# Kernel tuning notes

Measured on AMD Instinct MI355X. Metric: run time of the kernel, lower is better.

Reference implementation:

```python
import jax, jax.numpy as jnp
import numpy as np

T, B, H, W_IMG = 8, 4, 128, 128
NUM_CLS = 21
LEAK = 0.99   # config.leak_mem
THR = 1.0     # config.def_threshold
EPS = 1e-4    # BatchNorm2d eps


@jax.custom_vjp
def spike(mem):
    # Heaviside spike with 'Linear' surrogate gradient
    return (mem > THR).astype(mem.dtype)

def _spike_fwd(mem):
    return spike(mem), mem

def _spike_bwd(mem, g):
    # triangular (linear) surrogate around threshold
    return (g * jnp.maximum(0.0, 1.0 - jnp.abs(mem - THR)),)

spike.defvjp(_spike_fwd, _spike_bwd)


def conv(x, w, pad, dil=1):
    return jax.lax.conv_general_dilated(
        x, w, window_strides=(1, 1), padding=[(pad, pad), (pad, pad)],
        rhs_dilation=(dil, dil), dimension_numbers=('NCHW', 'OIHW', 'NCHW'))


def bn_apply(x, bn_t):
    # bn_t: [3, C] = (gamma, running_mean, running_var); bias=None in the model
    g, mu, var = bn_t[0], bn_t[1], bn_t[2]
    inv = (g / jnp.sqrt(var + EPS))[None, :, None, None]
    return (x - mu[None, :, None, None]) * inv


def avgpool(x):
    # AvgPool2d(kernel=3, stride=2, padding=1), count_include_pad=True -> /9
    s = jax.lax.reduce_window(x, 0.0, jax.lax.add, (1, 1, 3, 3), (1, 1, 2, 2),
                              [(0, 0), (0, 0), (1, 1), (1, 1)])
    return s / 9.0


def lif(x, w, bn_t, mem, pad, dil=1):
    # mem = leak*mem + BN_t(conv(x)); spike; soft reset by threshold
    out = bn_apply(conv(x, w, pad, dil), bn_t)
    mem = LEAK * mem + out
    s = spike(mem)
    return mem - THR * s, s


def _forward(x, u, W0, W1, W2, W3, W4, W5, W6, W7, W8,
             bn0, bn1, bn2, bn3, bn4, bn5, bn6, bn7):
    # Poisson generator: spike when u <= |x|, carrying sign of x. [T,B,3,H,W]
    spk_in = jnp.where(u <= jnp.abs(x)[None], jnp.sign(x)[None], 0.0)
    z = lambda c, h: jnp.zeros((B, c, h, h), x.dtype)
    init = (z(64, 128), z(64, 128), z(128, 64), z(128, 64),
            z(256, 32), z(256, 32), z(256, 32), z(1024, 32), z(NUM_CLS, 32))

    def step(carry, xs):
        m0, m1, m2, m3, m4, m5, m6, m7, macc = carry
        sp, b0, b1, b2, b3, b4, b5, b6, b7 = xs
        m0, o = lif(sp, W0, b0, m0, 1)
        m1, o = lif(o, W1, b1, m1, 1)
        o = avgpool(o)                      # 128 -> 64
        m2, o = lif(o, W2, b2, m2, 1)
        m3, o = lif(o, W3, b3, m3, 1)
        o = avgpool(o)                      # 64 -> 32
        m4, o = lif(o, W4, b4, m4, 1)
        m5, o = lif(o, W5, b5, m5, 2, 2)    # atrous256
        m6, o = lif(o, W6, b6, m6, 2, 2)    # atrous256
        m7, o = lif(o, W7, b7, m7, 12, 12)  # classifier atrous1024
        macc = macc + conv(o, W8, 0)        # output layer accumulates voltage
        return (m0, m1, m2, m3, m4, m5, m6, m7, macc), None

    carry, _ = jax.lax.scan(step, init, (spk_in, bn0, bn1, bn2, bn3, bn4, bn5, bn6, bn7))
    return carry[-1] / T


def setup_inputs() -> dict:
    key = jax.random.key(0)
    ks = jax.random.split(key, 24)

    def w(k, shape):
        fan_in = int(np.prod(shape[1:]))
        return jax.random.normal(k, shape, jnp.float32) / np.sqrt(fan_in)

    def bn(k, c):
        return jax.random.uniform(k, (T, 3, c), jnp.float32, 0.25, 1.25)

    inp = {
        'x': jax.random.normal(ks[0], (B, 3, H, W_IMG), jnp.float32),
        'u': jax.random.uniform(ks[1], (T, B, 3, H, W_IMG), jnp.float32),
        'W0': w(ks[2], (64, 3, 3, 3)),
        'W1': w(ks[3], (64, 64, 3, 3)),
        'W2': w(ks[4], (128, 64, 3, 3)),
        'W3': w(ks[5], (128, 128, 3, 3)),
        'W4': w(ks[6], (256, 128, 3, 3)),
        'W5': w(ks[7], (256, 256, 3, 3)),
        'W6': w(ks[8], (256, 256, 3, 3)),
        'W7': w(ks[9], (1024, 256, 3, 3)),
        'W8': w(ks[10], (NUM_CLS, 1024, 1, 1)),
        'bn0': bn(ks[11], 64), 'bn1': bn(ks[12], 64),
        'bn2': bn(ks[13], 128), 'bn3': bn(ks[14], 128),
        'bn4': bn(ks[15], 256), 'bn5': bn(ks[16], 256),
        'bn6': bn(ks[17], 256), 'bn7': bn(ks[18], 1024),
    }
    return inp


def reference(x, u, W0, W1, W2, W3, W4, W5, W6, W7, W8,
              bn0, bn1, bn2, bn3, bn4, bn5, bn6, bn7):
    return _forward(x, u, W0, W1, W2, W3, W4, W5, W6, W7, W8,
                    bn0, bn1, bn2, bn3, bn4, bn5, bn6, bn7)
```

## Files before the change

### kernel.cpp

```cpp
#include <hip/hip_runtime.h>
#include <hip/hip_bf16.h>
#include <cstddef>
#include <cstdint>

#define LEAK  0.99f
#define THRS  1.0f
#define BNEPS 1e-4f

static constexpr int TT   = 8;
static constexpr int BB   = 4;
static constexpr int NCLS = 21;

typedef __attribute__((ext_vector_type(8))) short short8v;
typedef __attribute__((ext_vector_type(4))) float f32x4;

__global__ void zero_f32(float* __restrict__ p, int n) {
  int i = blockIdx.x * blockDim.x + threadIdx.x;
  int stride = gridDim.x * blockDim.x;
  for (; i < n; i += stride) p[i] = 0.0f;
}

__global__ void scale_f32(float* __restrict__ p, int n, float s) {
  int i = blockIdx.x * blockDim.x + threadIdx.x;
  if (i < n) p[i] *= s;
}

__global__ void wsplit(const float* __restrict__ Wsrc,
                       __hip_bfloat16* __restrict__ whi, __hip_bfloat16* __restrict__ wlo,
                       int Co, int Ci, int Cip, float scale) {
  const int Kpad = 9 * Cip;
  const int n = Co * Kpad;
  int i = blockIdx.x * 256 + threadIdx.x;
  if (i >= n) return;
  int co = i / Kpad, k = i - co * Kpad;
  int tap = k / Cip, ci = k - tap * Cip;
  float w = 0.0f;
  if (ci < Ci) w = Wsrc[((size_t)co * Ci + ci) * 9 + tap] * scale;
  __hip_bfloat16 h = __float2bfloat16(w);
  float r = w - __bfloat162float(h);
  whi[i] = h;
  wlo[i] = __float2bfloat16(r);
}

__global__ void wsplit_l0(const float* __restrict__ W0,
                          __hip_bfloat16* __restrict__ whi, __hip_bfloat16* __restrict__ wlo) {
  int i = blockIdx.x * 256 + threadIdx.x;
  if (i >= 64 * 96) return;
  int co = i / 96, k = i - co * 96;
  int slot = k >> 3, ci = k & 7;
  float w = 0.0f;
  if (slot < 9 && ci < 3) w = W0[((size_t)co * 3 + ci) * 9 + slot];
  __hip_bfloat16 h = __float2bfloat16(w);
  float r = w - __bfloat162float(h);
  whi[i] = h;
  wlo[i] = __float2bfloat16(r);
}

__global__ void spike_gen8(const float* __restrict__ x, const float* __restrict__ u,
                           __hip_bfloat16* __restrict__ spk) {
  const int HW = 128 * 128;
  int i = blockIdx.x * 256 + threadIdx.x;
  if (i >= BB * HW) return;
  int b = i / HW, hw = i - b * HW;
  short8v o = {};
#pragma unroll
  for (int c = 0; c < 3; ++c) {
    float xv = x[((size_t)b * 3 + c) * HW + hw];
    float uv = u[((size_t)b * 3 + c) * HW + hw];
    float ax = fabsf(xv);
    float sg = (xv > 0.0f) ? 1.0f : ((xv < 0.0f) ? -1.0f : 0.0f);
    float s  = (uv <= ax) ? sg : 0.0f;
    __hip_bfloat16_raw raw = __hip_bfloat16_raw(__float2bfloat16(s));
    o[c] = (short)raw.x;
  }
  *(short8v*)(spk + (size_t)i * 8) = o;
}

__global__ __launch_bounds__(256) void gemm_lif_l0(
    const __hip_bfloat16* __restrict__ spk,
    const __hip_bfloat16* __restrict__ wsp,
    const float* __restrict__ bnt, float* __restrict__ mem,
    __hip_bfloat16* __restrict__ actout,
    const __hip_bfloat16* __restrict__ zp) {
  constexpr int M = 2, Co = 64, Kpk = 96, HW = 16384, H = 128, W = 128;
  __shared__ __hip_bfloat16 lds[3 * 64 * 32];
  const int lane = threadIdx.x & 63, wid = threadIdx.x >> 6;
  const int l15 = lane & 15, g = lane >> 4;

  const int nb = gridDim.x;
  const int flat = blockIdx.x;
  const int swz = (flat & 7) * (nb >> 3) + (flat >> 3);
  const int bx = swz & 511, by = swz >> 9;
  const int p0 = (bx * 4 + wid) * 32;
  const int co0 = by * 32;

  int b_[M], y_[M], x_[M];
#pragma unroll
  for (int m = 0; m < M; ++m) {
    int pb = p0 + m * 16;
    b_[m] = pb >> 14;
    int rem = pb & (HW - 1);
    y_[m] = rem >> 7;
    x_[m] = (rem & 127) + l15;
  }

  unsigned sgb[3];
#pragma unroll
  for (int i = 0; i < 3; ++i) {
    int f = wid * 48 + i * 16 + (lane >> 2);
    int cc = f >> 6;
    int r  = f & 63;
    int half = r >> 5;
    int co   = r & 31;
    int slot = (lane & 3) ^ ((co >> 1) & 3);
    sgb[i] = (unsigned)half * Co * Kpk + (unsigned)(co0 + co) * Kpk + slot * 8 + cc * 32;
  }
#pragma unroll
  for (int i = 0; i < 3; ++i) {
    const __hip_bfloat16* gp = wsp + sgb[i];
    __hip_bfloat16* lp = &lds[(wid * 48 + i * 16) * 32];
    __builtin_amdgcn_global_load_lds(
        (const __attribute__((address_space(1))) void*)gp,
        (__attribute__((address_space(3))) void*)lp, 16, 0, 0);
  }

  short8v aA[3][M];
#pragma unroll
  for (int c = 0; c < 3; ++c) {
    int tap = c * 4 + g;
    int ty = (tap * 11) >> 5;
    int tx = tap - ty * 3;
    int dy = ty - 1, dx = tx - 1;
#pragma unroll
    for (int m = 0; m < M; ++m) {
      int sy = y_[m] + dy, sx = x_[m] + dx;
      bool v = (tap < 9) & (sy >= 0) & (sy < H) & (sx >= 0) & (sx < W);
      int pix = (b_[m] << 14) + (sy << 7) + sx;
      const __hip_bfloat16* ap = v ? (spk + (size_t)pix * 8) : zp;
      aA[c][m] = *(const short8v*)ap;
    }
  }

  asm volatile("s_waitcnt vmcnt(%0)" :: "n"(6) : "memory");
  __builtin_amdgcn_s_barrier();
  __builtin_amdgcn_sched_barrier(0);

  f32x4 acc[M][2] = {};
  const int rdb = l15 * 32 + ((g ^ ((l15 >> 1) & 3)) * 8);
#pragma unroll
  for (int c = 0; c < 3; ++c) {
    short8v bh[2], bl[2];
#pragma unroll
    for (int j = 0; j < 2; ++j) {
      bh[j] = *(const short8v*)(&lds[c * 2048] + j * 512 + rdb);
      bl[j] = *(const short8v*)(&lds[c * 2048] + 1024 + j * 512 + rdb);
    }
    __builtin_amdgcn_s_setprio(1);
#pragma unroll
    for (int j = 0; j < 2; ++j)
#pragma unroll
      for (int m = 0; m < M; ++m) {
        acc[m][j] = __builtin_amdgcn_mfma_f32_16x16x32_bf16(aA[c][m], bh[j], acc[m][j], 0, 0, 0);
        acc[m][j] = __builtin_amdgcn_mfma_f32_16x16x32_bf16(aA[c][m], bl[j], acc[m][j], 0, 0, 0);
      }
    __builtin_amdgcn_s_setprio(0);
  }

#pragma unroll
  for (int j = 0; j < 2; ++j) {
    int c = co0 + j * 16 + l15;
    float ga = bnt[c], mu = bnt[Co + c], va = bnt[2 * Co + c];
    float sc = ga / sqrtf(va + BNEPS);
#pragma unroll
    for (int m = 0; m < M; ++m) {
      int pixb = p0 + m * 16 + 4 * g;
#pragma unroll
      for (int r = 0; r < 4; ++r) {
        size_t idx = (size_t)(pixb + r) * Co + c;
        float bno = (acc[m][j][r] - mu) * sc;
        float mv = LEAK * mem[idx] + bno;
        float s = (mv > THRS) ? 1.0f : 0.0f;
        actout[idx] = __float2bfloat16(s);
        mem[idx] = mv - s;
      }
    }
  }
}

template<int M, int N, int GRP, int CPT, int SPLIT>
__global__ __launch_bounds__(SPLIT * 256, 4) void gemm_lif(
    const __hip_bfloat16* __restrict__ actin,
    const __hip_bfloat16* __restrict__ wsp,
    const float* __restrict__ bnt,
    float* __restrict__ mem, __hip_bfloat16* __restrict__ actout,
    const __hip_bfloat16* __restrict__ zp,
    int Co, int lgHW, int lgW, int dil, int lgGX) {
  constexpr int NW = 4;
  constexpr int Cip = CPT * 32;
  constexpr int Kpad = 9 * Cip;
  constexpr int lgcpt = (CPT == 1) ? 0 : (CPT == 2) ? 1 : (CPT == 4) ? 2 : 3;
  constexpr int R  = N * 32;
  constexpr int lgR = (N == 1) ? 5 : ((N == 2) ? 6 : 7);
  constexpr int BUFROWS = GRP * R;
  constexpr int BUFELEM = BUFROWS * 32;
  constexpr int INSTS = BUFROWS / (16 * NW);
  constexpr int AM = M * GRP;
  constexpr int WAITN = AM;
  constexpr int NCH = (9 * CPT) / SPLIT;
  constexpr int NGRP = NCH / GRP;
  static_assert(NCH % GRP == 0, "group must divide per-half chunk count");
  __shared__ __hip_bfloat16 lds[SPLIT * 2 * BUFELEM];

  const int HW = 1 << lgHW, H = HW >> lgW, W = 1 << lgW;
  const unsigned CoKpad = (unsigned)Co * Kpad;
  const int lane = threadIdx.x & 63, wid = threadIdx.x >> 6;
  const int kw = wid >> 2;
  const int wq = wid & 3;
  const int l15 = lane & 15, g = lane >> 4;
  __hip_bfloat16* ldsh = lds + kw * 2 * BUFELEM;

  const int nb = gridDim.x;
  const int flat = blockIdx.x;
  const int swz = (flat & 7) * (nb >> 3) + (flat >> 3);
  const int bx = swz & ((1 << lgGX) - 1);
  const int by = swz >> lgGX;
  const int p0  = (bx * NW + wq) * (M * 16);
  const int co0 = by * (N * 16);

  int b_[M], y_[M], x_[M];
#pragma unroll
  for (int m = 0; m < M; ++m) {
    int pb = p0 + m * 16;
    b_[m] = pb >> lgHW;
    int rem = pb & (HW - 1);
    y_[m] = rem >> lgW;
    x_[m] = (rem & (W - 1)) + l15;
  }

  const unsigned kbase = (unsigned)kw * (NCH * 32);
  unsigned sgb[INSTS];
#pragma unroll
  for (int i = 0; i < INSTS; ++i) {
    int f  = wq * (BUFROWS / NW) + i * 16 + (lane >> 2);
    int cc = f >> lgR;
    int r  = f & (R - 1);
    int half = r >> (lgR - 1);
    int co   = r & (16 * N - 1);
    int slot = (lane & 3) ^ ((co >> 1) & 3);
    sgb[i] = (unsigned)half * CoKpad + (unsigned)(co0 + co) * Kpad + slot * 8
           + cc * 32 + kbase;
  }

  auto stage = [&](int gl, int buf) {
#pragma unroll
    for (int i = 0; i < INSTS; ++i) {
      const __hip_bfloat16* gp = wsp + sgb[i] + gl * (GRP * 32);
      __hip_bfloat16* lp = &ldsh[buf * BUFELEM + (wq * (BUFROWS / NW) + i * 16) * 32];
      __builtin_amdgcn_global_load_lds(
          (const __attribute__((address_space(1))) void*)gp,
          (__attribute__((address_space(3))) void*)lp, 16, 0, 0);
    }
  };

  const __hip_bfloat16* apc[M];
  auto mkaddr = [&](int tap) {
    int ty = (tap * 11) >> 5;
    int tx = tap - ty * 3;
    int dy = (ty - 1) * dil, dx = (tx - 1) * dil;
#pragma unroll
    for (int m = 0; m < M; ++m) {
      int sy = y_[m] + dy, sx = x_[m] + dx;
      bool v = (sy >= 0) & (sy < H) & (sx >= 0) & (sx < W);
      int pix = (b_[m] << lgHW) + (sy << lgW) + sx;
      apc[m] = v ? (actin + (size_t)pix * Cip + 8 * g) : (zp + 8 * g);
    }
  };

  auto prefA_slice = [&](int cg, int cc, short8v (&dst)[GRP][M], bool force) {
    if ((cg & (CPT - 1)) == 0 || force) mkaddr(cg >> lgcpt);
    int kc = (cg & (CPT - 1)) << 5;
#pragma unroll
    for (int m = 0; m < M; ++m)
      dst[cc][m] = *(const short8v*)(apc[m] + kc);
  };

  f32x4 acc[M][N] = {};
  const int rdb = l15 * 32 + ((g ^ ((l15 >> 1) & 3)) * 8);

  short8v aA[GRP][M], aB[GRP][M];

  auto grp_body = [&](int gi, short8v (&aU)[GRP][M], short8v (&aF)[GRP][M]) {
    asm volatile("s_waitcnt vmcnt(%0)" :: "n"(WAITN) : "memory");
    __builtin_amdgcn_s_barrier();
    __builtin_amdgcn_sched_barrier(0);

    const bool more = (gi + 1 < NGRP);
    if (more) stage(gi + 1, (gi + 1) & 1);

    const __hip_bfloat16* bp = &ldsh[(gi & 1) * BUFELEM];
#pragma unroll
    for (int cc = 0; cc < GRP; ++cc) {
      if (more) prefA_slice(kw * NCH + (gi + 1) * GRP + cc, cc, aF, false);
      short8v bh[N], bl[N];
#pragma unroll
      for (int j = 0; j < N; ++j) {
        bh[j] = *(const short8v*)(bp + cc * (R * 32) + j * 512 + rdb);
        bl[j] = *(const short8v*)(bp + cc * (R * 32) + (N * 512) + j * 512 + rdb);
      }
      __builtin_amdgcn_s_setprio(1);
#pragma unroll
      for (int j = 0; j < N; ++j)
#pragma unroll
        for (int m = 0; m < M; ++m) {
          acc[m][j] = __builtin_amdgcn_mfma_f32_16x16x32_bf16(aU[cc][m], bh[j], acc[m][j], 0, 0, 0);
          acc[m][j] = __builtin_amdgcn_mfma_f32_16x16x32_bf16(aU[cc][m], bl[j], acc[m][j], 0, 0, 0);
        }
      __builtin_amdgcn_s_setprio(0);
    }
  };

  stage(0, 0);
#pragma unroll
  for (int cc = 0; cc < GRP; ++cc)
    prefA_slice(kw * NCH + cc, cc, aA, cc == 0);

#pragma unroll
  for (int gi = 0; gi < NGRP; ++gi) {
    if (gi & 1) grp_body(gi, aB, aA);
    else        grp_body(gi, aA, aB);
  }

  if constexpr (SPLIT == 2) {
    asm volatile("s_waitcnt vmcnt(0) lgkmcnt(0)" ::: "memory");
    __builtin_amdgcn_s_barrier();
    float* red = (float*)lds;
    const int tid = wq * 64 + lane;
    if (kw == 1) {
#pragma unroll
      for (int m = 0; m < M; ++m)
#pragma unroll
        for (int j = 0; j < N; ++j)
#pragma unroll
          for (int r = 0; r < 4; ++r)
            red[((m * N + j) * 4 + r) * 256 + tid] = acc[m][j][r];
    }
    asm volatile("s_waitcnt lgkmcnt(0)" ::: "memory");
    __builtin_amdgcn_s_barrier();
    if (kw == 1) return;
#pragma unroll
    for (int m = 0; m < M; ++m)
#pragma unroll
      for (int j = 0; j < N; ++j)
#pragma unroll
        for (int r = 0; r < 4; ++r)
          acc[m][j][r] += red[((m * N + j) * 4 + r) * 256 + tid];
  }

#pragma unroll
  for (int j = 0; j < N; ++j) {
    int c = co0 + j * 16 + l15;
    float ga = bnt[c], mu = bnt[Co + c], va = bnt[2 * Co + c];
    float sc = ga / sqrtf(va + BNEPS);
#pragma unroll
    for (int m = 0; m < M; ++m) {
      int pixb = p0 + m * 16 + 4 * g;
#pragma unroll
      for (int r = 0; r < 4; ++r) {
        size_t idx = (size_t)(pixb + r) * Co + c;
        float bno = (acc[m][j][r] - mu) * sc;
        float mv = LEAK * mem[idx] + bno;
        float s = (mv > THRS) ? 1.0f : 0.0f;
        actout[idx] = __float2bfloat16(s);
        mem[idx] = mv - s;
      }
    }
  }
}

__global__ void avgpool_sum8(const __hip_bfloat16* __restrict__ in,
                             __hip_bfloat16* __restrict__ out, int C, int H, int W) {
  const int Ho = H >> 1, Wo = W >> 1;
  const int C8 = C >> 3;
  const int n = BB * Ho * Wo * C8;
  int i = blockIdx.x * 256 + threadIdx.x;
  if (i >= n) return;
  int c8 = i % C8; int t = i / C8;
  int xo = t % Wo; t /= Wo;
  int yo = t % Ho; int b = t / Ho;
  const int y0 = 2 * yo - 1, x0 = 2 * xo - 1;
  float s[8] = {0, 0, 0, 0, 0, 0, 0, 0};
#pragma unroll
  for (int dy = 0; dy < 3; ++dy) {
    int iy = y0 + dy;
    if (iy < 0 || iy >= H) continue;
#pragma unroll
    for (int dx = 0; dx < 3; ++dx) {
      int ix = x0 + dx;
      if (ix < 0 || ix >= W) continue;
      short8v v = *(const short8v*)(in + (((size_t)b * H + iy) * W + ix) * C + c8 * 8);
#pragma unroll
      for (int e = 0; e < 8; ++e) {
        __hip_bfloat16_raw raw; raw.x = (unsigned short)v[e];
        s[e] += __bfloat162float(__hip_bfloat16(raw));
      }
    }
  }
  short8v o;
#pragma unroll
  for (int e = 0; e < 8; ++e) {
    __hip_bfloat16_raw raw = __hip_bfloat16_raw(__float2bfloat16(s[e]));
    o[e] = (short)raw.x;
  }
  *(short8v*)(out + (size_t)i * 8) = o;
}

__global__ void out_conv(const __hip_bfloat16* __restrict__ act,
                         const float* __restrict__ W8, float* __restrict__ out) {
  int gw = (blockIdx.x * 256 + threadIdx.x) >> 6;
  int lane = threadIdx.x & 63;
  int b = gw >> 10, pix = gw & 1023;
  const __hip_bfloat16* ap = act + ((size_t)gw << 10);
  float acc[NCLS];
#pragma unroll
  for (int c = 0; c < NCLS; ++c) acc[c] = 0.0f;
  for (int j = 0; j < 16; ++j) {
    int ci = j * 64 + lane;
    float av = __bfloat162float(ap[ci]);
#pragma unroll
    for (int c = 0; c < NCLS; ++c) acc[c] = fmaf(av, W8[c * 1024 + ci], acc[c]);
  }
#pragma unroll
  for (int c = 0; c < NCLS; ++c) {
    float v = acc[c];
    for (int off = 32; off; off >>= 1) v += __shfl_xor(v, off, 64);
    if (lane == 0) out[((size_t)b * NCLS + c) * 1024 + pix] += v;
  }
}

extern "C" void kernel_launch(void* const* d_in, const int* in_sizes, int n_in,
                              void* d_out, int out_size, void* d_ws, size_t ws_size,
                              hipStream_t stream) {
  const float* x = (const float*)d_in[0];
  const float* u = (const float*)d_in[1];
  const float* Wc[9];
  for (int i = 0; i < 9; ++i) Wc[i] = (const float*)d_in[2 + i];
  const float* bn[8];
  for (int i = 0; i < 8; ++i) bn[i] = (const float*)d_in[11 + i];

  const int Ci_[8]  = {3, 64, 64, 128, 128, 256, 256, 256};
  const int Cip_[8] = {8, 64, 64, 128, 128, 256, 256, 256};
  const int Co_[8]  = {64, 64, 128, 128, 256, 256, 256, 1024};
  const int HH_[8]  = {128, 128, 64, 64, 32, 32, 32, 32};
  const float wsc_[8] = {1.f, 1.f, 1.f / 9.f, 1.f, 1.f / 9.f, 1.f, 1.f, 1.f};

  float* ws = (float*)d_ws;
  size_t off = 0;
  auto align8 = [](size_t v) { return (v + 7) & ~(size_t)7; };

  float* memp[8];
  for (int i = 0; i < 8; ++i) {
    memp[i] = ws + off;
    off += (size_t)BB * HH_[i] * HH_[i] * Co_[i];
  }
  __hip_bfloat16* zp = (__hip_bfloat16*)(ws + off);
  off += 256;
  const size_t zero_floats = off;
  __hip_bfloat16* spk = (__hip_bfloat16*)(ws + off);
  off += (size_t)BB * 16384 * 8 / 2;
  __hip_bfloat16* actA = (__hip_bfloat16*)(ws + off); off += 2097152;
  __hip_bfloat16* actB = (__hip_bfloat16*)(ws + off); off += 2097152;
  __hip_bfloat16* wall[8];
  wall[0] = (__hip_bfloat16*)(ws + off);
  off = align8(off + (size_t)64 * 96);
  for (int i = 1; i < 8; ++i) {
    size_t n = (size_t)Co_[i] * 9 * Cip_[i];
    wall[i] = (__hip_bfloat16*)(ws + off);
    off = align8(off + n);
  }

  zero_f32<<<2048, 256, 0, stream>>>(ws, (int)zero_floats);
  zero_f32<<<(BB * NCLS * 1024 + 255) / 256, 256, 0, stream>>>((float*)d_out, BB * NCLS * 1024);

  wsplit_l0<<<(64 * 96 + 255) / 256, 256, 0, stream>>>(Wc[0], wall[0], wall[0] + 64 * 96);
  for (int i = 1; i < 8; ++i) {
    int n = Co_[i] * 9 * Cip_[i];
    wsplit<<<(n + 255) / 256, 256, 0, stream>>>(Wc[i], wall[i], wall[i] + n,
                                                Co_[i], Ci_[i], Cip_[i], wsc_[i]);
  }

  const size_t uT = (size_t)BB * 3 * 16384;
  for (int t = 0; t < TT; ++t) {
    spike_gen8<<<(BB * 16384 + 255) / 256, 256, 0, stream>>>(x, u + (size_t)t * uT, spk);
    gemm_lif_l0<<<1024, 256, 0, stream>>>(spk, wall[0], bn[0] + (size_t)t * 3 * 64, memp[0], actA, zp);
    gemm_lif<2, 2, 3, 2, 1><<<1024, 256, 0, stream>>>(actA, wall[1], bn[1] + (size_t)t * 3 * 64,   memp[1], actB, zp, 64,   14, 7, 1, 9);
    avgpool_sum8<<<(BB * 64 * 64 * 8 + 255) / 256, 256, 0, stream>>>(actB, actA, 64, 128, 128);
    gemm_lif<2, 2, 3, 2, 2><<<512, 512, 0, stream>>>(actA, wall[2], bn[2] + (size_t)t * 3 * 128,  memp[2], actB, zp, 128,  12, 6, 1, 7);
    gemm_lif<2, 2, 3, 4, 2><<<512, 512, 0, stream>>>(actB, wall[3], bn[3] + (size_t)t * 3 * 128,  memp[3], actA, zp, 128,  12, 6, 1, 7);
    avgpool_sum8<<<(BB * 32 * 32 * 16 + 255) / 256, 256, 0, stream>>>(actA, actB, 128, 64, 64);
    gemm_lif<1, 2, 3, 4, 2><<<512, 512, 0, stream>>>(actB, wall[4], bn[4] + (size_t)t * 3 * 256,   memp[4], actA, zp, 256,  10, 5, 1, 6);
    gemm_lif<1, 2, 4, 8, 2><<<512, 512, 0, stream>>>(actA, wall[5], bn[5] + (size_t)t * 3 * 256,   memp[5], actB, zp, 256,  10, 5, 2, 6);
    gemm_lif<1, 2, 4, 8, 2><<<512, 512, 0, stream>>>(actB, wall[6], bn[6] + (size_t)t * 3 * 256,   memp[6], actA, zp, 256,  10, 5, 2, 6);
    gemm_lif<2, 4, 2, 8, 2><<<512, 512, 0, stream>>>(actA, wall[7], bn[7] + (size_t)t * 3 * 1024, memp[7], actB, zp, 1024, 10, 5, 12, 5);
    out_conv<<<dim3(BB * 1024 / 4), 256, 0, stream>>>(actB, Wc[8], (float*)d_out);
  }
  scale_f32<<<(BB * NCLS * 1024 + 255) / 256, 256, 0, stream>>>((float*)d_out, BB * NCLS * 1024, 1.0f / TT);
}
```

Before: 1.908 ms.

## Move time loop inside layer kernels and keep LIF membrane state in registers

Each layer now runs as one launch per layer that loops over all timesteps internally, instead of one launch per layer per timestep. The membrane potential stays in registers across timesteps, so the fp32 membrane buffers in global memory are no longer read and written. Spike generation, pooling and the output conv are batched over time, and the final averaging is folded into the output conv. In exchange, activation buffers grow to hold every timestep, and each block serialises the timestep loop, so there is less parallelism per launch.

Result: slower. 2.222 ms (+16.4%).

```diff
diff --git a/kernel.cpp b/kernel.cpp
--- a/kernel.cpp
+++ b/kernel.cpp
@@ -18,11 +18,6 @@
   int i = blockIdx.x * blockDim.x + threadIdx.x;
   int stride = gridDim.x * blockDim.x;
   for (; i < n; i += stride) p[i] = 0.0f;
-}
-
-__global__ void scale_f32(float* __restrict__ p, int n, float s) {
-  int i = blockIdx.x * blockDim.x + threadIdx.x;
-  if (i < n) p[i] *= s;
 }
 
 __global__ void wsplit(const float* __restrict__ Wsrc,
@@ -58,15 +53,17 @@
 
 __global__ void spike_gen8(const float* __restrict__ x, const float* __restrict__ u,
                            __hip_bfloat16* __restrict__ spk) {
-  const int HW = 128 * 128;
+  const int HW = 16384;
   int i = blockIdx.x * 256 + threadIdx.x;
-  if (i >= BB * HW) return;
-  int b = i / HW, hw = i - b * HW;
+  if (i >= TT * BB * HW) return;
+  int hw = i & (HW - 1);
+  int tb = i >> 14;
+  int b  = tb & 3;
   short8v o = {};
 #pragma unroll
   for (int c = 0; c < 3; ++c) {
-    float xv = x[((size_t)b * 3 + c) * HW + hw];
-    float uv = u[((size_t)b * 3 + c) * HW + hw];
+    float xv = x[((b * 3 + c) << 14) + hw];
+    float uv = u[(((size_t)tb * 3 + c) << 14) + hw];
     float ax = fabsf(xv);
     float sg = (xv > 0.0f) ? 1.0f : ((xv < 0.0f) ? -1.0f : 0.0f);
     float s  = (uv <= ax) ? sg : 0.0f;
@@ -79,7 +76,7 @@
 __global__ __launch_bounds__(256) void gemm_lif_l0(
     const __hip_bfloat16* __restrict__ spk,
     const __hip_bfloat16* __restrict__ wsp,
-    const float* __restrict__ bnt, float* __restrict__ mem,
+    const float* __restrict__ bnt,
     __hip_bfloat16* __restrict__ actout,
     const __hip_bfloat16* __restrict__ zp) {
   constexpr int M = 2, Co = 64, Kpk = 96, HW = 16384, H = 128, W = 128;
@@ -124,7 +121,7 @@
         (__attribute__((address_space(3))) void*)lp, 16, 0, 0);
   }
 
-  short8v aA[3][M];
+  int poff[3][M]; bool pval[3][M];
 #pragma unroll
   for (int c = 0; c < 3; ++c) {
     int tap = c * 4 + g;
@@ -134,54 +131,69 @@
 #pragma unroll
     for (int m = 0; m < M; ++m) {
       int sy = y_[m] + dy, sx = x_[m] + dx;
-      bool v = (tap < 9) & (sy >= 0) & (sy < H) & (sx >= 0) & (sx < W);
-      int pix = (b_[m] << 14) + (sy << 7) + sx;
-      const __hip_bfloat16* ap = v ? (spk + (size_t)pix * 8) : zp;
-      aA[c][m] = *(const short8v*)ap;
-    }
-  }
-
-  asm volatile("s_waitcnt vmcnt(%0)" :: "n"(6) : "memory");
+      pval[c][m] = (tap < 9) & (sy >= 0) & (sy < H) & (sx >= 0) & (sx < W);
+      poff[c][m] = (b_[m] << 14) + (sy << 7) + sx;
+    }
+  }
+
+  asm volatile("s_waitcnt vmcnt(0)" ::: "memory");
   __builtin_amdgcn_s_barrier();
-  __builtin_amdgcn_sched_barrier(0);
-
-  f32x4 acc[M][2] = {};
+
   const int rdb = l15 * 32 + ((g ^ ((l15 >> 1) & 3)) * 8);
-#pragma unroll
-  for (int c = 0; c < 3; ++c) {
-    short8v bh[2], bl[2];
+  short8v bh[3][2], bl[3][2];
+#pragma unroll
+  for (int c = 0; c < 3; ++c)
 #pragma unroll
     for (int j = 0; j < 2; ++j) {
-      bh[j] = *(const short8v*)(&lds[c * 2048] + j * 512 + rdb);
-      bl[j] = *(const short8v*)(&lds[c * 2048] + 1024 + j * 512 + rdb);
-    }
-    __builtin_amdgcn_s_setprio(1);
-#pragma unroll
-    for (int j = 0; j < 2; ++j)
+      bh[c][j] = *(const short8v*)(&lds[c * 2048] + j * 512 + rdb);
+      bl[c][j] = *(const short8v*)(&lds[c * 2048] + 1024 + j * 512 + rdb);
+    }
+
+  f32x4 memv[M][2] = {};
+#pragma unroll 1
+  for (int t = 0; t < TT; ++t) {
+    const __hip_bfloat16* st = spk + (size_t)t * (BB * HW * 8);
+    short8v aA[3][M];
+#pragma unroll
+    for (int c = 0; c < 3; ++c)
 #pragma unroll
       for (int m = 0; m < M; ++m) {
-        acc[m][j] = __builtin_amdgcn_mfma_f32_16x16x32_bf16(aA[c][m], bh[j], acc[m][j], 0, 0, 0);
-        acc[m][j] = __builtin_amdgcn_mfma_f32_16x16x32_bf16(aA[c][m], bl[j], acc[m][j], 0, 0, 0);
-      }
-    __builtin_amdgcn_s_setprio(0);
-  }
-
-#pragma unroll
-  for (int j = 0; j < 2; ++j) {
-    int c = co0 + j * 16 + l15;
-    float ga = bnt[c], mu = bnt[Co + c], va = bnt[2 * Co + c];
-    float sc = ga / sqrtf(va + BNEPS);
-#pragma unroll
-    for (int m = 0; m < M; ++m) {
-      int pixb = p0 + m * 16 + 4 * g;
-#pragma unroll
-      for (int r = 0; r < 4; ++r) {
-        size_t idx = (size_t)(pixb + r) * Co + c;
-        float bno = (acc[m][j][r] - mu) * sc;
-        float mv = LEAK * mem[idx] + bno;
-        float s = (mv > THRS) ? 1.0f : 0.0f;
-        actout[idx] = __float2bfloat16(s);
-        mem[idx] = mv - s;
+        const __hip_bfloat16* ap = pval[c][m] ? (st + (size_t)poff[c][m] * 8) : zp;
+        aA[c][m] = *(const short8v*)ap;
+      }
+
+    f32x4 acc[M][2] = {};
+#pragma unroll
+    for (int c = 0; c < 3; ++c) {
+      __builtin_amdgcn_s_setprio(1);
+#pragma unroll
+      for (int j = 0; j < 2; ++j)
+#pragma unroll
+        for (int m = 0; m < M; ++m) {
+          acc[m][j] = __builtin_amdgcn_mfma_f32_16x16x32_bf16(aA[c][m], bh[c][j], acc[m][j], 0, 0, 0);
+          acc[m][j] = __builtin_amdgcn_mfma_f32_16x16x32_bf16(aA[c][m], bl[c][j], acc[m][j], 0, 0, 0);
+        }
+      __builtin_amdgcn_s_setprio(0);
+    }
+
+    const float* bt = bnt + t * 3 * Co;
+#pragma unroll
+    for (int j = 0; j < 2; ++j) {
+      int c = co0 + j * 16 + l15;
+      float ga = bt[c], mu = bt[Co + c], va = bt[2 * Co + c];
+      float sc = ga / sqrtf(va + BNEPS);
+#pragma unroll
+      for (int m = 0; m < M; ++m) {
+        int pixb = p0 + m * 16 + 4 * g;
+#pragma unroll
+        for (int r = 0; r < 4; ++r) {
+          size_t idx = (size_t)t * (BB * HW * Co) + (size_t)(pixb + r) * Co + c;
+          float bno = (acc[m][j][r] - mu) * sc;
+          float mv = LEAK * memv[m][j][r] + bno;
+          float s = (mv > THRS) ? 1.0f : 0.0f;
+          actout[idx] = __float2bfloat16(s);
+          memv[m][j][r] = mv - s;
+        }
       }
     }
   }
@@ -192,7 +204,7 @@
     const __hip_bfloat16* __restrict__ actin,
     const __hip_bfloat16* __restrict__ wsp,
     const float* __restrict__ bnt,
-    float* __restrict__ mem, __hip_bfloat16* __restrict__ actout,
+    __hip_bfloat16* __restrict__ actout,
     const __hip_bfloat16* __restrict__ zp,
     int Co, int lgHW, int lgW, int dil, int lgGX) {
   constexpr int NW = 4;
@@ -262,6 +274,10 @@
     }
   };
 
+  const size_t astride = (size_t)(BB << lgHW) * Cip;
+  const size_t ostride = (size_t)(BB << lgHW) * Co;
+  const __hip_bfloat16* actt = actin;
+
   const __hip_bfloat16* apc[M];
   auto mkaddr = [&](int tap) {
     int ty = (tap * 11) >> 5;
@@ -272,7 +288,7 @@
       int sy = y_[m] + dy, sx = x_[m] + dx;
       bool v = (sy >= 0) & (sy < H) & (sx >= 0) & (sx < W);
       int pix = (b_[m] << lgHW) + (sy << lgW) + sx;
-      apc[m] = v ? (actin + (size_t)pix * Cip + 8 * g) : (zp + 8 * g);
+      apc[m] = v ? (actt + (size_t)pix * Cip + 8 * g) : (zp + 8 * g);
     }
   };
 
@@ -284,10 +300,10 @@
       dst[cc][m] = *(const short8v*)(apc[m] + kc);
   };
 
-  f32x4 acc[M][N] = {};
   const int rdb = l15 * 32 + ((g ^ ((l15 >> 1) & 3)) * 8);
-
   short8v aA[GRP][M], aB[GRP][M];
+  f32x4 acc[M][N];
+  f32x4 memv[M][N] = {};
 
   auto grp_body = [&](int gi, short8v (&aU)[GRP][M], short8v (&aF)[GRP][M]) {
     asm volatile("s_waitcnt vmcnt(%0)" :: "n"(WAITN) : "memory");
@@ -319,69 +335,87 @@
     }
   };
 
-  stage(0, 0);
-#pragma unroll
-  for (int cc = 0; cc < GRP; ++cc)
-    prefA_slice(kw * NCH + cc, cc, aA, cc == 0);
-
-#pragma unroll
-  for (int gi = 0; gi < NGRP; ++gi) {
-    if (gi & 1) grp_body(gi, aB, aA);
-    else        grp_body(gi, aA, aB);
-  }
-
-  if constexpr (SPLIT == 2) {
-    asm volatile("s_waitcnt vmcnt(0) lgkmcnt(0)" ::: "memory");
-    __builtin_amdgcn_s_barrier();
-    float* red = (float*)lds;
-    const int tid = wq * 64 + lane;
-    if (kw == 1) {
-#pragma unroll
-      for (int m = 0; m < M; ++m)
-#pragma unroll
-        for (int j = 0; j < N; ++j)
-#pragma unroll
-          for (int r = 0; r < 4; ++r)
-            red[((m * N + j) * 4 + r) * 256 + tid] = acc[m][j][r];
-    }
+#pragma unroll 1
+  for (int t = 0; t < TT; ++t) {
+    actt = actin + (size_t)t * astride;
+#pragma unroll
+    for (int m = 0; m < M; ++m)
+#pragma unroll
+      for (int j = 0; j < N; ++j) acc[m][j] = f32x4{0.f, 0.f, 0.f, 0.f};
+
+    stage(0, 0);
+#pragma unroll
+    for (int cc = 0; cc < GRP; ++cc)
+      prefA_slice(kw * NCH + cc, cc, aA, cc == 0);
+
+#pragma unroll
+    for (int gi = 0; gi < NGRP; ++gi) {
+      if (gi & 1) grp_body(gi, aB, aA);
+      else        grp_body(gi, aA, aB);
+    }
+
+    if constexpr (SPLIT == 2) {
+      asm volatile("s_waitcnt vmcnt(0) lgkmcnt(0)" ::: "memory");
+      __builtin_amdgcn_s_barrier();
+      float* red = (float*)lds;
+      const int tid = wq * 64 + lane;
+      if (kw == 1) {
+#pragma unroll
+        for (int m = 0; m < M; ++m)
+#pragma unroll
+          for (int j = 0; j < N; ++j)
+#pragma unroll
+            for (int r = 0; r < 4; ++r)
+              red[((m * N + j) * 4 + r) * 256 + tid] = acc[m][j][r];
+      }
+      asm volatile("s_waitcnt lgkmcnt(0)" ::: "memory");
+      __builtin_amdgcn_s_barrier();
+      __builtin_amdgcn_sched_barrier(0);
+      if (kw == 0) {
+#pragma unroll
+        for (int m = 0; m < M; ++m)
+#pragma unroll
+          for (int j = 0; j < N; ++j)
+#pragma unroll
+            for (int r = 0; r < 4; ++r)
+              acc[m][j][r] += red[((m * N + j) * 4 + r) * 256 + tid];
+      }
+    }
+
+    if (kw == 0) {
+      const float* bt = bnt + t * 3 * Co;
+#pragma unroll
+      for (int j = 0; j < N; ++j) {
+        int c = co0 + j * 16 + l15;
+        float ga = bt[c], mu = bt[Co + c], va = bt[2 * Co + c];
+        float sc = ga / sqrtf(va + BNEPS);
+#pragma unroll
+        for (int m = 0; m < M; ++m) {
+          int pixb = p0 + m * 16 + 4 * g;
+#pragma unroll
+          for (int r = 0; r < 4; ++r) {
+            size_t idx = (size_t)t * ostride + (size_t)(pixb + r) * Co + c;
+            float bno = (acc[m][j][r] - mu) * sc;
+            float mv = LEAK * memv[m][j][r] + bno;
+            float s = (mv > THRS) ? 1.0f : 0.0f;
+            actout[idx] = __float2bfloat16(s);
+            memv[m][j][r] = mv - s;
+          }
+        }
+      }
+    }
+
     asm volatile("s_waitcnt lgkmcnt(0)" ::: "memory");
     __builtin_amdgcn_s_barrier();
-    if (kw == 1) return;
-#pragma unroll
-    for (int m = 0; m < M; ++m)
-#pragma unroll
-      for (int j = 0; j < N; ++j)
-#pragma unroll
-        for (int r = 0; r < 4; ++r)
-          acc[m][j][r] += red[((m * N + j) * 4 + r) * 256 + tid];
-  }
-
-#pragma unroll
-  for (int j = 0; j < N; ++j) {
-    int c = co0 + j * 16 + l15;
-    float ga = bnt[c], mu = bnt[Co + c], va = bnt[2 * Co + c];
-    float sc = ga / sqrtf(va + BNEPS);
-#pragma unroll
-    for (int m = 0; m < M; ++m) {
-      int pixb = p0 + m * 16 + 4 * g;
-#pragma unroll
-      for (int r = 0; r < 4; ++r) {
-        size_t idx = (size_t)(pixb + r) * Co + c;
-        float bno = (acc[m][j][r] - mu) * sc;
-        float mv = LEAK * mem[idx] + bno;
-        float s = (mv > THRS) ? 1.0f : 0.0f;
-        actout[idx] = __float2bfloat16(s);
-        mem[idx] = mv - s;
-      }
-    }
+    __builtin_amdgcn_sched_barrier(0);
   }
 }
 
 __global__ void avgpool_sum8(const __hip_bfloat16* __restrict__ in,
-                             __hip_bfloat16* __restrict__ out, int C, int H, int W) {
+                             __hip_bfloat16* __restrict__ out, int NB, int C, int H, int W) {
   const int Ho = H >> 1, Wo = W >> 1;
   const int C8 = C >> 3;
-  const int n = BB * Ho * Wo * C8;
+  const int n = NB * Ho * Wo * C8;
   int i = blockIdx.x * 256 + threadIdx.x;
   if (i >= n) return;
   int c8 = i % C8; int t = i / C8;
@@ -419,21 +453,24 @@
   int gw = (blockIdx.x * 256 + threadIdx.x) >> 6;
   int lane = threadIdx.x & 63;
   int b = gw >> 10, pix = gw & 1023;
-  const __hip_bfloat16* ap = act + ((size_t)gw << 10);
   float acc[NCLS];
 #pragma unroll
   for (int c = 0; c < NCLS; ++c) acc[c] = 0.0f;
-  for (int j = 0; j < 16; ++j) {
-    int ci = j * 64 + lane;
-    float av = __bfloat162float(ap[ci]);
-#pragma unroll
-    for (int c = 0; c < NCLS; ++c) acc[c] = fmaf(av, W8[c * 1024 + ci], acc[c]);
+#pragma unroll 1
+  for (int t = 0; t < TT; ++t) {
+    const __hip_bfloat16* ap = act + (((size_t)t * 4096 + gw) << 10);
+    for (int j = 0; j < 16; ++j) {
+      int ci = j * 64 + lane;
+      float av = __bfloat162float(ap[ci]);
+#pragma unroll
+      for (int c = 0; c < NCLS; ++c) acc[c] = fmaf(av, W8[c * 1024 + ci], acc[c]);
+    }
   }
 #pragma unroll
   for (int c = 0; c < NCLS; ++c) {
     float v = acc[c];
     for (int off = 32; off; off >>= 1) v += __shfl_xor(v, off, 64);
-    if (lane == 0) out[((size_t)b * NCLS + c) * 1024 + pix] += v;
+    if (lane == 0) out[((size_t)b * NCLS + c) * 1024 + pix] = v * (1.0f / TT);
   }
 }
 
@@ -450,25 +487,19 @@
   const int Ci_[8]  = {3, 64, 64, 128, 128, 256, 256, 256};
   const int Cip_[8] = {8, 64, 64, 128, 128, 256, 256, 256};
   const int Co_[8]  = {64, 64, 128, 128, 256, 256, 256, 1024};
-  const int HH_[8]  = {128, 128, 64, 64, 32, 32, 32, 32};
   const float wsc_[8] = {1.f, 1.f, 1.f / 9.f, 1.f, 1.f / 9.f, 1.f, 1.f, 1.f};
 
   float* ws = (float*)d_ws;
   size_t off = 0;
   auto align8 = [](size_t v) { return (v + 7) & ~(size_t)7; };
 
-  float* memp[8];
-  for (int i = 0; i < 8; ++i) {
-    memp[i] = ws + off;
-    off += (size_t)BB * HH_[i] * HH_[i] * Co_[i];
-  }
-  __hip_bfloat16* zp = (__hip_bfloat16*)(ws + off);
-  off += 256;
-  const size_t zero_floats = off;
+  __hip_bfloat16* zp = (__hip_bfloat16*)(ws + off); off += 256;
   __hip_bfloat16* spk = (__hip_bfloat16*)(ws + off);
-  off += (size_t)BB * 16384 * 8 / 2;
-  __hip_bfloat16* actA = (__hip_bfloat16*)(ws + off); off += 2097152;
-  __hip_bfloat16* actB = (__hip_bfloat16*)(ws + off); off += 2097152;
+  off += (size_t)TT * BB * 16384 * 8 / 2;
+  __hip_bfloat16* P = (__hip_bfloat16*)(ws + off);
+  off += (size_t)TT * BB * 16384 * 64 / 2;
+  __hip_bfloat16* Q = (__hip_bfloat16*)(ws + off);
+  off += (size_t)TT * BB * 16384 * 64 / 2;
   __hip_bfloat16* wall[8];
   wall[0] = (__hip_bfloat16*)(ws + off);
   off = align8(off + (size_t)64 * 96);
@@ -478,8 +509,7 @@
     off = align8(off + n);
   }
 
-  zero_f32<<<2048, 256, 0, stream>>>(ws, (int)zero_floats);
-  zero_f32<<<(BB * NCLS * 1024 + 255) / 256, 256, 0, stream>>>((float*)d_out, BB * NCLS * 1024);
+  zero_f32<<<1, 256, 0, stream>>>(ws, 256);
 
   wsplit_l0<<<(64 * 96 + 255) / 256, 256, 0, stream>>>(Wc[0], wall[0], wall[0] + 64 * 96);
   for (int i = 1; i < 8; ++i) {
@@ -488,20 +518,16 @@
                                                 Co_[i], Ci_[i], Cip_[i], wsc_[i]);
   }
 
-  const size_t uT = (size_t)BB * 3 * 16384;
-  for (int t = 0; t < TT; ++t) {
-    spike_gen8<<<(BB * 16384 + 255) / 256, 256, 0, stream>>>(x, u + (size_t)t * uT, spk);
-    gemm_lif_l0<<<1024, 256, 0, stream>>>(spk, wall[0], bn[0] + (size_t)t * 3 * 64, memp[0], actA, zp);
-    gemm_lif<2, 2, 3, 2, 1><<<1024, 256, 0, stream>>>(actA, wall[1], bn[1] + (size_t)t * 3 * 64,   memp[1], actB, zp, 64,   14, 7, 1, 9);
-    avgpool_sum8<<<(BB * 64 * 64 * 8 + 255) / 256, 256, 0, stream>>>(actB, actA, 64, 128, 128);
-    gemm_lif<2, 2, 3, 2, 2><<<512, 512, 0, stream>>>(actA, wall[2], bn[2] + (size_t)t * 3 * 128,  memp[2], actB, zp, 128,  12, 6, 1, 7);
-    gemm_lif<2, 2, 3, 4, 2><<<512, 512, 0, stream>>>(actB, wall[3], bn[3] + (size_t)t * 3 * 128,  memp[3], actA, zp, 128,  12, 6, 1, 7);
-    avgpool_sum8<<<(BB * 32 * 32 * 16 + 255) / 256, 256, 0, stream>>>(actA, actB, 128, 64, 64);
-    gemm_lif<1, 2, 3, 4, 2><<<512, 512, 0, stream>>>(actB, wall[4], bn[4] + (size_t)t * 3 * 256,   memp[4], actA, zp, 256,  10, 5, 1, 6);
-    gemm_lif<1, 2, 4, 8, 2><<<512, 512, 0, stream>>>(actA, wall[5], bn[5] + (size_t)t * 3 * 256,   memp[5], actB, zp, 256,  10, 5, 2, 6);
-    gemm_lif<1, 2, 4, 8, 2><<<512, 512, 0, stream>>>(actB, wall[6], bn[6] + (size_t)t * 3 * 256,   memp[6], actA, zp, 256,  10, 5, 2, 6);
-    gemm_lif<2, 4, 2, 8, 2><<<512, 512, 0, stream>>>(actA, wall[7], bn[7] + (size_t)t * 3 * 1024, memp[7], actB, zp, 1024, 10, 5, 12, 5);
-    out_conv<<<dim3(BB * 1024 / 4), 256, 0, stream>>>(actB, Wc[8], (float*)d_out);
-  }
-  scale_f32<<<(BB * NCLS * 1024 + 255) / 256, 256, 0, stream>>>((float*)d_out, BB * NCLS * 1024, 1.0f / TT);
-}
+  spike_gen8<<<(TT * BB * 16384 + 255) / 256, 256, 0, stream>>>(x, u, spk);
+  gemm_lif_l0<<<1024, 256, 0, stream>>>(spk, wall[0], bn[0], P, zp);
+  gemm_lif<2, 2, 3, 2, 1><<<1024, 256, 0, stream>>>(P, wall[1], bn[1], Q, zp, 64, 14, 7, 1, 9);
+  avgpool_sum8<<<(TT * BB * 64 * 64 * 8 + 255) / 256, 256, 0, stream>>>(Q, P, TT * BB, 64, 128, 128);
+  gemm_lif<2, 2, 3, 2, 2><<<512, 512, 0, stream>>>(P, wall[2], bn[2], Q, zp, 128, 12, 6, 1, 7);
+  gemm_lif<2, 2, 3, 4, 2><<<512, 512, 0, stream>>>(Q, wall[3], bn[3], P, zp, 128, 12, 6, 1, 7);
+  avgpool_sum8<<<(TT * BB * 32 * 32 * 16 + 255) / 256, 256, 0, stream>>>(P, Q, TT * BB, 128, 64, 64);
+  gemm_lif<1, 2, 3, 4, 2><<<512, 512, 0, stream>>>(Q, wall[4], bn[4], P, zp, 256, 10, 5, 1, 6);
+  gemm_lif<1, 2, 4, 8, 2><<<512, 512, 0, stream>>>(P, wall[5], bn[5], Q, zp, 256, 10, 5, 2, 6);
+  gemm_lif<1, 2, 4, 8, 2><<<512, 512, 0, stream>>>(Q, wall[6], bn[6], P, zp, 256, 10, 5, 2, 6);
+  gemm_lif<2, 4, 2, 8, 2><<<512, 512, 0, stream>>>(P, wall[7], bn[7], Q, zp, 1024, 10, 5, 12, 5);
+  out_conv<<<1024, 256, 0, stream>>>(Q, Wc[8], (float*)d_out);
+}
```

## Use 32x32x16 MFMA tiles for M==2 conv configurations

Applied to the files above, without the earlier changes.

Adds a separate compute path for the M==2 conv kernel instantiations that uses 32x32x16 bf16 MFMA instructions instead of pairs of 16x16x32 ones. A-operand addressing, LDS B-fragment reads, the split-K reduction and the fused BN/LIF epilogue are all remapped to the 32-row accumulator layout. The aim is fewer MFMA issues and more operand reuse per instruction. In exchange the addressing and layout mapping become more complex, and the K-slot swizzle has to match the staged weight layout.

Measured after the change: 1.957 ms. +2.5%, slower.

```diff
diff --git a/kernel.cpp b/kernel.cpp
--- a/kernel.cpp
+++ b/kernel.cpp
@@ -13,6 +13,7 @@
 
 typedef __attribute__((ext_vector_type(8))) short short8v;
 typedef __attribute__((ext_vector_type(4))) float f32x4;
+typedef __attribute__((ext_vector_type(16))) float f32x16;
 
 __global__ void zero_f32(float* __restrict__ p, int n) {
   int i = blockIdx.x * blockDim.x + threadIdx.x;
@@ -216,7 +217,6 @@
   const int lane = threadIdx.x & 63, wid = threadIdx.x >> 6;
   const int kw = wid >> 2;
   const int wq = wid & 3;
-  const int l15 = lane & 15, g = lane >> 4;
   __hip_bfloat16* ldsh = lds + kw * 2 * BUFELEM;
 
   const int nb = gridDim.x;
@@ -226,16 +226,6 @@
   const int by = swz >> lgGX;
   const int p0  = (bx * NW + wq) * (M * 16);
   const int co0 = by * (N * 16);
-
-  int b_[M], y_[M], x_[M];
-#pragma unroll
-  for (int m = 0; m < M; ++m) {
-    int pb = p0 + m * 16;
-    b_[m] = pb >> lgHW;
-    int rem = pb & (HW - 1);
-    y_[m] = rem >> lgW;
-    x_[m] = (rem & (W - 1)) + l15;
-  }
 
   const unsigned kbase = (unsigned)kw * (NCH * 32);
   unsigned sgb[INSTS];
@@ -262,112 +252,242 @@
     }
   };
 
-  const __hip_bfloat16* apc[M];
-  auto mkaddr = [&](int tap) {
-    int ty = (tap * 11) >> 5;
-    int tx = tap - ty * 3;
-    int dy = (ty - 1) * dil, dx = (tx - 1) * dil;
+  if constexpr (M == 1) {
+    const int l15 = lane & 15, g = lane >> 4;
+
+    int b_[M], y_[M], x_[M];
 #pragma unroll
     for (int m = 0; m < M; ++m) {
-      int sy = y_[m] + dy, sx = x_[m] + dx;
+      int pb = p0 + m * 16;
+      b_[m] = pb >> lgHW;
+      int rem = pb & (HW - 1);
+      y_[m] = rem >> lgW;
+      x_[m] = (rem & (W - 1)) + l15;
+    }
+
+    const __hip_bfloat16* apc[M];
+    auto mkaddr = [&](int tap) {
+      int ty = (tap * 11) >> 5;
+      int tx = tap - ty * 3;
+      int dy = (ty - 1) * dil, dx = (tx - 1) * dil;
+#pragma unroll
+      for (int m = 0; m < M; ++m) {
+        int sy = y_[m] + dy, sx = x_[m] + dx;
+        bool v = (sy >= 0) & (sy < H) & (sx >= 0) & (sx < W);
+        int pix = (b_[m] << lgHW) + (sy << lgW) + sx;
+        apc[m] = v ? (actin + (size_t)pix * Cip + 8 * g) : (zp + 8 * g);
+      }
+    };
+
+    auto prefA_slice = [&](int cg, int cc, short8v (&dst)[GRP][M], bool force) {
+      if ((cg & (CPT - 1)) == 0 || force) mkaddr(cg >> lgcpt);
+      int kc = (cg & (CPT - 1)) << 5;
+#pragma unroll
+      for (int m = 0; m < M; ++m)
+        dst[cc][m] = *(const short8v*)(apc[m] + kc);
+    };
+
+    f32x4 acc[M][N] = {};
+    const int rdb = l15 * 32 + ((g ^ ((l15 >> 1) & 3)) * 8);
+
+    short8v aA[GRP][M], aB[GRP][M];
+
+    auto grp_body = [&](int gi, short8v (&aU)[GRP][M], short8v (&aF)[GRP][M]) {
+      asm volatile("s_waitcnt vmcnt(%0)" :: "n"(WAITN) : "memory");
+      __builtin_amdgcn_s_barrier();
+      __builtin_amdgcn_sched_barrier(0);
+
+      const bool more = (gi + 1 < NGRP);
+      if (more) stage(gi + 1, (gi + 1) & 1);
+
+      const __hip_bfloat16* bp = &ldsh[(gi & 1) * BUFELEM];
+#pragma unroll
+      for (int cc = 0; cc < GRP; ++cc) {
+        if (more) prefA_slice(kw * NCH + (gi + 1) * GRP + cc, cc, aF, false);
+        short8v bh[N], bl[N];
+#pragma unroll
+        for (int j = 0; j < N; ++j) {
+          bh[j] = *(const short8v*)(bp + cc * (R * 32) + j * 512 + rdb);
+          bl[j] = *(const short8v*)(bp + cc * (R * 32) + (N * 512) + j * 512 + rdb);
+        }
+        __builtin_amdgcn_s_setprio(1);
+#pragma unroll
+        for (int j = 0; j < N; ++j)
+#pragma unroll
+          for (int m = 0; m < M; ++m) {
+            acc[m][j] = __builtin_amdgcn_mfma_f32_16x16x32_bf16(aU[cc][m], bh[j], acc[m][j], 0, 0, 0);
+            acc[m][j] = __builtin_amdgcn_mfma_f32_16x16x32_bf16(aU[cc][m], bl[j], acc[m][j], 0, 0, 0);
+          }
+        __builtin_amdgcn_s_setprio(0);
+      }
+    };
+
+    stage(0, 0);
+#pragma unroll
+    for (int cc = 0; cc < GRP; ++cc)
+      prefA_slice(kw * NCH + cc, cc, aA, cc == 0);
+
+#pragma unroll
+    for (int gi = 0; gi < NGRP; ++gi) {
+      if (gi & 1) grp_body(gi, aB, aA);
+      else        grp_body(gi, aA, aB);
+    }
+
+    if constexpr (SPLIT == 2) {
+      asm volatile("s_waitcnt vmcnt(0) lgkmcnt(0)" ::: "memory");
+      __builtin_amdgcn_s_barrier();
+      float* red = (float*)lds;
+      const int tid = wq * 64 + lane;
+      if (kw == 1) {
+#pragma unroll
+        for (int m = 0; m < M; ++m)
+#pragma unroll
+          for (int j = 0; j < N; ++j)
+#pragma unroll
+            for (int r = 0; r < 4; ++r)
+              red[((m * N + j) * 4 + r) * 256 + tid] = acc[m][j][r];
+      }
+      asm volatile("s_waitcnt lgkmcnt(0)" ::: "memory");
+      __builtin_amdgcn_s_barrier();
+      if (kw == 1) return;
+#pragma unroll
+      for (int m = 0; m < M; ++m)
+#pragma unroll
+        for (int j = 0; j < N; ++j)
+#pragma unroll
+          for (int r = 0; r < 4; ++r)
+            acc[m][j][r] += red[((m * N + j) * 4 + r) * 256 + tid];
+    }
+
+#pragma unroll
+    for (int j = 0; j < N; ++j) {
+      int c = co0 + j * 16 + l15;
+      float ga = bnt[c], mu = bnt[Co + c], va = bnt[2 * Co + c];
+      float sc = ga / sqrtf(va + BNEPS);
+#pragma unroll
+      for (int m = 0; m < M; ++m) {
+        int pixb = p0 + m * 16 + 4 * g;
+#pragma unroll
+        for (int r = 0; r < 4; ++r) {
+          size_t idx = (size_t)(pixb + r) * Co + c;
+          float bno = (acc[m][j][r] - mu) * sc;
+          float mv = LEAK * mem[idx] + bno;
+          float s = (mv > THRS) ? 1.0f : 0.0f;
+          actout[idx] = __float2bfloat16(s);
+          mem[idx] = mv - s;
+        }
+      }
+    }
+  } else {
+    static_assert(M == 2 && (N % 2) == 0, "M32 path requires M==2, even N");
+    constexpr int NR = N / 2;
+    const int l31 = lane & 31, h5 = lane >> 5;
+    const int bkey = (l31 >> 1) & 3;
+
+    int b0_, y0_, x0_;
+    {
+      int rem = p0 & (HW - 1);
+      b0_ = p0 >> lgHW;
+      y0_ = rem >> lgW;
+      x0_ = (rem & (W - 1)) + l31;
+    }
+
+    const __hip_bfloat16* apc32;
+    auto mkaddr = [&](int tap) {
+      int ty = (tap * 11) >> 5;
+      int tx = tap - ty * 3;
+      int dy = (ty - 1) * dil, dx = (tx - 1) * dil;
+      int sy = y0_ + dy, sx = x0_ + dx;
       bool v = (sy >= 0) & (sy < H) & (sx >= 0) & (sx < W);
-      int pix = (b_[m] << lgHW) + (sy << lgW) + sx;
-      apc[m] = v ? (actin + (size_t)pix * Cip + 8 * g) : (zp + 8 * g);
-    }
-  };
-
-  auto prefA_slice = [&](int cg, int cc, short8v (&dst)[GRP][M], bool force) {
-    if ((cg & (CPT - 1)) == 0 || force) mkaddr(cg >> lgcpt);
-    int kc = (cg & (CPT - 1)) << 5;
-#pragma unroll
-    for (int m = 0; m < M; ++m)
-      dst[cc][m] = *(const short8v*)(apc[m] + kc);
-  };
-
-  f32x4 acc[M][N] = {};
-  const int rdb = l15 * 32 + ((g ^ ((l15 >> 1) & 3)) * 8);
-
-  short8v aA[GRP][M], aB[GRP][M];
-
-  auto grp_body = [&](int gi, short8v (&aU)[GRP][M], short8v (&aF)[GRP][M]) {
-    asm volatile("s_waitcnt vmcnt(%0)" :: "n"(WAITN) : "memory");
-    __builtin_amdgcn_s_barrier();
-    __builtin_amdgcn_sched_barrier(0);
-
-    const bool more = (gi + 1 < NGRP);
-    if (more) stage(gi + 1, (gi + 1) & 1);
-
-    const __hip_bfloat16* bp = &ldsh[(gi & 1) * BUFELEM];
-#pragma unroll
-    for (int cc = 0; cc < GRP; ++cc) {
-      if (more) prefA_slice(kw * NCH + (gi + 1) * GRP + cc, cc, aF, false);
-      short8v bh[N], bl[N];
-#pragma unroll
-      for (int j = 0; j < N; ++j) {
-        bh[j] = *(const short8v*)(bp + cc * (R * 32) + j * 512 + rdb);
-        bl[j] = *(const short8v*)(bp + cc * (R * 32) + (N * 512) + j * 512 + rdb);
-      }
-      __builtin_amdgcn_s_setprio(1);
-#pragma unroll
-      for (int j = 0; j < N; ++j)
-#pragma unroll
-        for (int m = 0; m < M; ++m) {
-          acc[m][j] = __builtin_amdgcn_mfma_f32_16x16x32_bf16(aU[cc][m], bh[j], acc[m][j], 0, 0, 0);
-          acc[m][j] = __builtin_amdgcn_mfma_f32_16x16x32_bf16(aU[cc][m], bl[j], acc[m][j], 0, 0, 0);
+      int pix = (b0_ << lgHW) + (sy << lgW) + sx;
+      apc32 = v ? (actin + (size_t)pix * Cip + 8 * h5) : (zp + 8 * h5);
+    };
+
+    auto prefA_slice = [&](int cg, int cc, short8v (&dst)[GRP][2], bool force) {
+      if ((cg & (CPT - 1)) == 0 || force) mkaddr(cg >> lgcpt);
+      int kc = (cg & (CPT - 1)) << 5;
+      dst[cc][0] = *(const short8v*)(apc32 + kc);
+      dst[cc][1] = *(const short8v*)(apc32 + kc + 16);
+    };
+
+    f32x16 acc[NR] = {};
+    short8v aA[GRP][2], aB[GRP][2];
+
+    auto grp_body = [&](int gi, short8v (&aU)[GRP][2], short8v (&aF)[GRP][2]) {
+      asm volatile("s_waitcnt vmcnt(%0)" :: "n"(WAITN) : "memory");
+      __builtin_amdgcn_s_barrier();
+      __builtin_amdgcn_sched_barrier(0);
+
+      const bool more = (gi + 1 < NGRP);
+      if (more) stage(gi + 1, (gi + 1) & 1);
+
+      const __hip_bfloat16* bp = &ldsh[(gi & 1) * BUFELEM];
+#pragma unroll
+      for (int cc = 0; cc < GRP; ++cc) {
+        if (more) prefA_slice(kw * NCH + (gi + 1) * GRP + cc, cc, aF, false);
+#pragma unroll
+        for (int kh = 0; kh < 2; ++kh) {
+          const int pslot = ((kh * 2 + h5) ^ bkey) * 8;
+          short8v bh[NR], bl[NR];
+#pragma unroll
+          for (int j = 0; j < NR; ++j) {
+            bh[j] = *(const short8v*)(bp + cc * (R * 32) + (j * 32 + l31) * 32 + pslot);
+            bl[j] = *(const short8v*)(bp + cc * (R * 32) + (16 * N + j * 32 + l31) * 32 + pslot);
+          }
+          __builtin_amdgcn_s_setprio(1);
+#pragma unroll
+          for (int j = 0; j < NR; ++j) {
+            acc[j] = __builtin_amdgcn_mfma_f32_32x32x16_bf16(aU[cc][kh], bh[j], acc[j], 0, 0, 0);
+            acc[j] = __builtin_amdgcn_mfma_f32_32x32x16_bf16(aU[cc][kh], bl[j], acc[j], 0, 0, 0);
+          }
+          __builtin_amdgcn_s_setprio(0);
         }
-      __builtin_amdgcn_s_setprio(0);
-    }
-  };
-
-  stage(0, 0);
-#pragma unroll
-  for (int cc = 0; cc < GRP; ++cc)
-    prefA_slice(kw * NCH + cc, cc, aA, cc == 0);
-
-#pragma unroll
-  for (int gi = 0; gi < NGRP; ++gi) {
-    if (gi & 1) grp_body(gi, aB, aA);
-    else        grp_body(gi, aA, aB);
-  }
-
-  if constexpr (SPLIT == 2) {
-    asm volatile("s_waitcnt vmcnt(0) lgkmcnt(0)" ::: "memory");
-    __builtin_amdgcn_s_barrier();
-    float* red = (float*)lds;
-    const int tid = wq * 64 + lane;
-    if (kw == 1) {
-#pragma unroll
-      for (int m = 0; m < M; ++m)
-#pragma unroll
-        for (int j = 0; j < N; ++j)
-#pragma unroll
-          for (int r = 0; r < 4; ++r)
-            red[((m * N + j) * 4 + r) * 256 + tid] = acc[m][j][r];
-    }
-    asm volatile("s_waitcnt lgkmcnt(0)" ::: "memory");
-    __builtin_amdgcn_s_barrier();
-    if (kw == 1) return;
-#pragma unroll
-    for (int m = 0; m < M; ++m)
-#pragma unroll
-      for (int j = 0; j < N; ++j)
-#pragma unroll
-        for (int r = 0; r < 4; ++r)
-          acc[m][j][r] += red[((m * N + j) * 4 + r) * 256 + tid];
-  }
-
-#pragma unroll
-  for (int j = 0; j < N; ++j) {
-    int c = co0 + j * 16 + l15;
-    float ga = bnt[c], mu = bnt[Co + c], va = bnt[2 * Co + c];
-    float sc = ga / sqrtf(va + BNEPS);
-#pragma unroll
-    for (int m = 0; m < M; ++m) {
-      int pixb = p0 + m * 16 + 4 * g;
-#pragma unroll
-      for (int r = 0; r < 4; ++r) {
-        size_t idx = (size_t)(pixb + r) * Co + c;
-        float bno = (acc[m][j][r] - mu) * sc;
+      }
+    };
+
+    stage(0, 0);
+#pragma unroll
+    for (int cc = 0; cc < GRP; ++cc)
+      prefA_slice(kw * NCH + cc, cc, aA, cc == 0);
+
+#pragma unroll
+    for (int gi = 0; gi < NGRP; ++gi) {
+      if (gi & 1) grp_body(gi, aB, aA);
+      else        grp_body(gi, aA, aB);
+    }
+
+    if constexpr (SPLIT == 2) {
+      asm volatile("s_waitcnt vmcnt(0) lgkmcnt(0)" ::: "memory");
+      __builtin_amdgcn_s_barrier();
+      float* red = (float*)lds;
+      const int tid = wq * 64 + lane;
+      if (kw == 1) {
+#pragma unroll
+        for (int j = 0; j < NR; ++j)
+#pragma unroll
+          for (int r = 0; r < 16; ++r)
+            red[(j * 16 + r) * 256 + tid] = acc[j][r];
+      }
+      asm volatile("s_waitcnt lgkmcnt(0)" ::: "memory");
+      __builtin_amdgcn_s_barrier();
+      if (kw == 1) return;
+#pragma unroll
+      for (int j = 0; j < NR; ++j)
+#pragma unroll
+        for (int r = 0; r < 16; ++r)
+          acc[j][r] += red[(j * 16 + r) * 256 + tid];
+    }
+
+#pragma unroll
+    for (int j = 0; j < NR; ++j) {
+      int c = co0 + j * 32 + l31;
+      float ga = bnt[c], mu = bnt[Co + c], va = bnt[2 * Co + c];
+      float sc = ga / sqrtf(va + BNEPS);
+#pragma unroll
+      for (int r = 0; r < 16; ++r) {
+        int pixel = p0 + (r & 3) + 8 * (r >> 2) + 4 * h5;
+        size_t idx = (size_t)pixel * Co + c;
+        float bno = (acc[j][r] - mu) * sc;
         float mv = LEAK * mem[idx] + bno;
         float s = (mv > THRS) ? 1.0f : 0.0f;
         actout[idx] = __float2bfloat16(s);
```
